# Optimization experiments

Measured on AMD Instinct MI355X. Metric: run time of the kernel, lower is better.

## Reference

```python
import jax, jax.numpy as jnp
import numpy as np

EPS = 1e-5
K_NN = 16

def _lin1d(x, W, b):
    # 1x1 Conv1d: x (B,C,N) -> (B,O,N)
    return jnp.einsum('oc,bcn->bon', W, x) + b[None, :, None]

def _lin2d(x, W, b):
    # 1x1 Conv2d: x (B,C,N,K) -> (B,O,N,K)
    return jnp.einsum('oc,bcnk->bonk', W, x) + b[None, :, None, None]

def _bn2d(x, gamma, beta):
    # train-mode BatchNorm2d over (B, N, K) per channel
    mean = jnp.mean(x, axis=(0, 2, 3), keepdims=True)
    var = jnp.var(x, axis=(0, 2, 3), keepdims=True)
    xh = (x - mean) * jax.lax.rsqrt(var + EPS)
    return gamma[None, :, None, None] * xh + beta[None, :, None, None]

def _knn_idx(pq, ps, k):
    # pq (B,3,N), ps (B,3,M) -> idx (B,N,K) of k nearest support points
    d2 = (jnp.sum(pq * pq, axis=1)[:, :, None]
          + jnp.sum(ps * ps, axis=1)[:, None, :]
          - 2.0 * jnp.einsum('bcn,bcm->bnm', pq, ps))
    _, idx = jax.lax.top_k(-d2, k)
    return idx

def _group(x, idx):
    # x (B,C,M), idx (B,N,K) -> (B,C,N,K)
    return jnp.take_along_axis(x[:, :, None, :], idx[:, None, :, :], axis=3)

def setup_inputs() -> dict:
    key = jax.random.key(0)
    ks = jax.random.split(key, 20)
    B, C, D, N, M, H = 4, 128, 64, 2048, 2048, 256
    s = lambda k, shape, scale: (jax.random.normal(k, shape, dtype=jnp.float32) * scale)
    return {
        'pq': s(ks[0], (B, 3, N), 1.0),
        'fq': s(ks[1], (B, C, N), 1.0),
        'ps': s(ks[2], (B, 3, M), 1.0),
        'fs': s(ks[3], (B, C, M), 1.0),
        'Wq': s(ks[4], (D, C), 0.05), 'bq': jnp.zeros((D,), jnp.float32),
        'Wk': s(ks[5], (D, C), 0.05), 'bk': jnp.zeros((D,), jnp.float32),
        'Wv': s(ks[6], (D, C), 0.05), 'bv': jnp.zeros((D,), jnp.float32),
        'Wp1': s(ks[7], (D, 3), 0.2), 'bp1': jnp.zeros((D,), jnp.float32),
        'gp': jnp.ones((D,), jnp.float32), 'btp': jnp.zeros((D,), jnp.float32),
        'Wp2': s(ks[8], (D, D), 0.05), 'bp2': jnp.zeros((D,), jnp.float32),
        'Wa1': s(ks[9], (H, D), 0.05), 'ba1': jnp.zeros((H,), jnp.float32),
        'ga': jnp.ones((H,), jnp.float32), 'bta': jnp.zeros((H,), jnp.float32),
        'Wa2': s(ks[10], (D, H), 0.05), 'ba2': jnp.zeros((D,), jnp.float32),
        'We': s(ks[11], (C, D), 0.05), 'be': jnp.zeros((C,), jnp.float32),
    }

def reference(pq, fq, ps, fs, Wq, bq, Wk, bk, Wv, bv,
              Wp1, bp1, gp, btp, Wp2, bp2,
              Wa1, ba1, ga, bta, Wa2, ba2, We, be):
    identity = fq
    q = _lin1d(fq, Wq, bq)          # (B,D,N)
    k = _lin1d(fs, Wk, bk)          # (B,D,M)
    v = _lin1d(fs, Wv, bv)          # (B,D,M)
    idx = _knn_idx(pq, ps, K_NN)    # (B,N,K)
    key_g = _group(k, idx)          # (B,D,N,K)
    qk_rel = q[:, :, :, None] - key_g
    pos_rel = pq[:, :, :, None] - _group(ps, idx)  # (B,3,N,K)
    # pos_mlp: conv-bn-relu-conv
    pe = _lin2d(pos_rel, Wp1, bp1)
    pe = jax.nn.relu(_bn2d(pe, gp, btp))
    pe = _lin2d(pe, Wp2, bp2)       # (B,D,N,K)
    # attn_mlp: conv-bn-relu-conv
    a = _lin2d(qk_rel + pe, Wa1, ba1)
    a = jax.nn.relu(_bn2d(a, ga, bta))
    a = _lin2d(a, Wa2, ba2)         # (B,D,N,K)
    attn = jax.nn.softmax(a, axis=-1)
    val = _group(v, idx) + pe       # (B,D,N,K)
    agg = jnp.einsum('bcnk,bcnk->bcn', attn, val)
    return _lin1d(agg, We, be) + identity
```

## Files before the change

### kernel.cpp

```cpp
#include <hip/hip_runtime.h>
#include <stdint.h>

#define NN 2048
#define MM 2048
#define NSAMP 131072

typedef float  fv4 __attribute__((ext_vector_type(4)));
typedef short  bfv8 __attribute__((ext_vector_type(8)));
typedef short  bfv4 __attribute__((ext_vector_type(4)));
typedef unsigned short u16;
typedef unsigned long long u64;

__device__ inline u16 f2bf(float x){
  unsigned u = __float_as_uint(x);
  return (u16)((u + 0x7FFFu + ((u>>16)&1u)) >> 16);
}
__device__ inline float bf2f(u16 u){ return __uint_as_float(((unsigned)u)<<16); }
#define MFMA16 __builtin_amdgcn_mfma_f32_16x16x32_bf16

__global__ __launch_bounds__(256) void k_prep(
    const float* __restrict__ Wq, const float* __restrict__ Wk, const float* __restrict__ Wv,
    const float* __restrict__ Wp2, const float* __restrict__ Wa2, const float* __restrict__ We,
    const float* __restrict__ ps,
    u16* __restrict__ Wqbf, u16* __restrict__ Wkbf, u16* __restrict__ Wvbf,
    u16* __restrict__ Wp2bf, u16* __restrict__ Wa2bf, u16* __restrict__ Webf,
    fv4* __restrict__ psP) {
  int gid = blockIdx.x * 256 + threadIdx.x;
  if (gid < 8192)  { Wqbf[gid] = f2bf(Wq[gid]); Wkbf[gid] = f2bf(Wk[gid]);
                     Wvbf[gid] = f2bf(Wv[gid]); Webf[gid] = f2bf(We[gid]); }
  if (gid < 4096)  Wp2bf[gid] = f2bf(Wp2[gid]);
  if (gid < 16384) Wa2bf[gid] = f2bf(Wa2[gid]);
  if (gid < 8192)  { int b = gid >> 11, m = gid & 2047;
    float x = ps[(b*3+0)*MM + m], y = ps[(b*3+1)*MM + m], z = ps[(b*3+2)*MM + m];
    fv4 p; p.x = x; p.y = y; p.z = z; p.w = x*x + y*y + z*z;
    psP[gid] = p; }
}

__global__ __launch_bounds__(256) void k_qkv(
    const float* __restrict__ fq, const float* __restrict__ fs,
    const u16* __restrict__ Wqbf, const u16* __restrict__ Wkbf, const u16* __restrict__ Wvbf,
    const float* __restrict__ bq, const float* __restrict__ bk, const float* __restrict__ bv,
    float* __restrict__ qT, float* __restrict__ kT, float* __restrict__ vT) {
  __shared__ u16 tile[2][32 * 136];
  int bid = blockIdx.x;
  int b = bid >> 6, p0 = (bid & 63) * 32;
  int t = threadIdx.x;
  int w = t >> 6, l = t & 63, lq = l >> 4, ln = l & 15;
  {
    int cq = t >> 3, n4 = (t & 7) * 4;
    #pragma unroll
    for (int it = 0; it < 4; ++it) {
      int c = it * 32 + cq;
      fv4 vq = *(const fv4*)&fq[(b*128 + c)*2048 + p0 + n4];
      fv4 vs = *(const fv4*)&fs[(b*128 + c)*2048 + p0 + n4];
      #pragma unroll
      for (int j = 0; j < 4; ++j) {
        tile[0][(n4 + j)*136 + c] = f2bf(vq[j]);
        tile[1][(n4 + j)*136 + c] = f2bf(vs[j]);
      }
    }
  }
  bfv8 A[3][4];
  #pragma unroll
  for (int mat = 0; mat < 3; ++mat) {
    const u16* W = mat == 0 ? Wqbf : (mat == 1 ? Wkbf : Wvbf);
    #pragma unroll
    for (int kk = 0; kk < 4; ++kk)
      A[mat][kk] = *(const bfv8*)(W + (w*16 + ln)*128 + kk*32 + lq*8);
  }
  __syncthreads();
  fv4 acc[3][2];
  #pragma unroll
  for (int mat = 0; mat < 3; ++mat) {
    const u16* tl = tile[mat == 0 ? 0 : 1];
    #pragma unroll
    for (int nt = 0; nt < 2; ++nt) {
      fv4 a = {0.f,0.f,0.f,0.f};
      #pragma unroll
      for (int kk = 0; kk < 4; ++kk) {
        bfv8 bb = *(const bfv8*)&tl[(nt*16 + ln)*136 + kk*32 + lq*8];
        a = MFMA16(A[mat][kk], bb, a, 0, 0, 0);
      }
      acc[mat][nt] = a;
    }
  }
  #pragma unroll
  for (int mat = 0; mat < 3; ++mat) {
    float* dst = mat == 0 ? qT : (mat == 1 ? kT : vT);
    const float* bia = mat == 0 ? bq : (mat == 1 ? bk : bv);
    fv4 bq4 = *(const fv4*)&bia[w*16 + lq*4];
    #pragma unroll
    for (int nt = 0; nt < 2; ++nt) {
      fv4 o = acc[mat][nt] + bq4;
      *(fv4*)&dst[(b*NN + p0 + nt*16 + ln)*64 + w*16 + lq*4] = o;
    }
  }
}

__global__ __launch_bounds__(128) void k_knn(
    const float* __restrict__ pq, const fv4* __restrict__ psP,
    int* __restrict__ idxb, float* __restrict__ posPart) {
  __shared__ u64 cand[2][64 * 17];
  __shared__ float sacc[2][9];
  int t = threadIdx.x, w = t >> 6, lane = t & 63;
  int qi = blockIdx.x * 2 + w;
  int b = qi >> 11, n = qi & 2047;
  const float* pqb = pq + b * 3 * NN;
  const fv4* psb = psP + b * 2048;
  float qx = pqb[n], qy = pqb[NN + n], qz = pqb[2 * NN + n];
  float qq = qx * qx + qy * qy + qz * qz;

  u64 A[16], Bv[16];
  #pragma unroll
  for (int j = 0; j < 16; ++j) {
    int m = lane + 64 * j;
    fv4 P = psb[m];
    float d2 = qq + P.w - 2.f * (qx * P.x + qy * P.y + qz * P.z);
    unsigned bu = __float_as_uint(d2);
    bu = (bu & 0x80000000u) ? ~bu : (bu | 0x80000000u);
    A[j] = (((u64)bu) << 32) | (unsigned)m;
  }
  #pragma unroll
  for (int j = 0; j < 16; ++j) {
    int m = lane + 64 * (j + 16);
    fv4 P = psb[m];
    float d2 = qq + P.w - 2.f * (qx * P.x + qy * P.y + qz * P.z);
    unsigned bu = __float_as_uint(d2);
    bu = (bu & 0x80000000u) ? ~bu : (bu | 0x80000000u);
    Bv[j] = (((u64)bu) << 32) | (unsigned)m;
  }
  #pragma unroll
  for (int k = 2; k <= 16; k <<= 1) {
    #pragma unroll
    for (int j = k >> 1; j > 0; j >>= 1) {
      #pragma unroll
      for (int i = 0; i < 16; ++i) {
        int l2 = i ^ j;
        if (l2 > i) {
          bool up = ((i & k) == 0);
          { u64 x = A[i], y = A[l2];
            bool sw = up ? (y < x) : (x < y);
            A[i] = sw ? y : x;  A[l2] = sw ? x : y; }
          { u64 x = Bv[i], y = Bv[l2];
            bool sw = up ? (y < x) : (x < y);
            Bv[i] = sw ? y : x; Bv[l2] = sw ? x : y; }
        }
      }
    }
  }
  #pragma unroll
  for (int i = 0; i < 16; ++i) {
    u64 y = Bv[15 - i];
    A[i] = A[i] < y ? A[i] : y;
  }
  #pragma unroll
  for (int j = 8; j > 0; j >>= 1) {
    #pragma unroll
    for (int i = 0; i < 16; ++i) {
      int l2 = i ^ j;
      if (l2 > i) {
        u64 x = A[i], y = A[l2];
        bool sw = (y < x);
        A[i] = sw ? y : x;  A[l2] = sw ? x : y;
      }
    }
  }
  #pragma unroll
  for (int i = 0; i < 16; ++i) cand[w][lane * 17 + i] = A[i];
  float s0=0.f,s1=0.f,s2=0.f,s3=0.f,s4=0.f,s5=0.f,s6=0.f,s7=0.f,s8=0.f;
  int head = 0;
  for (int r = 0; r < 16; ++r) {
    u64 v = (head < 16) ? cand[w][lane * 17 + head] : ~0ULL;
    u64 mv = v;
    #pragma unroll
    for (int off = 32; off > 0; off >>= 1) {
      u64 o = __shfl_xor(mv, off, 64);
      mv = o < mv ? o : mv;
    }
    if (v == mv) head++;
    unsigned m = (unsigned)(mv & 0xFFFFFFFFu);
    if (lane == 0) idxb[qi * 16 + r] = (int)m;
    fv4 P = psb[m];
    float r0 = qx - P.x, r1 = qy - P.y, r2 = qz - P.z;
    s0 += r0; s1 += r1; s2 += r2;
    s3 += r0*r0; s4 += r0*r1; s5 += r0*r2;
    s6 += r1*r1; s7 += r1*r2; s8 += r2*r2;
  }
  if (lane == 0) {
    sacc[w][0]=s0; sacc[w][1]=s1; sacc[w][2]=s2; sacc[w][3]=s3; sacc[w][4]=s4;
    sacc[w][5]=s5; sacc[w][6]=s6; sacc[w][7]=s7; sacc[w][8]=s8;
  }
  __syncthreads();
  if (t < 9) posPart[blockIdx.x * 12 + t] = sacc[0][t] + sacc[1][t];
}

__global__ __launch_bounds__(256) void k_posfinal(
    const float* __restrict__ Wp1, const float* __restrict__ bp1,
    const float* __restrict__ gp, const float* __restrict__ btp,
    const float* __restrict__ posPart, float* __restrict__ Wp1f, float* __restrict__ bp1f) {
  __shared__ float red[4][9];
  __shared__ float st[9];
  int t = threadIdx.x;
  int w = t >> 6, lane = t & 63;
  float s[9];
  #pragma unroll
  for (int i = 0; i < 9; ++i) s[i] = 0.f;
  #pragma unroll
  for (int it = 0; it < 16; ++it) {
    const float* p = posPart + (it * 256 + t) * 12;
    fv4 a = *(const fv4*)p;
    fv4 b4 = *(const fv4*)(p + 4);
    float c8 = p[8];
    s[0]+=a.x; s[1]+=a.y; s[2]+=a.z; s[3]+=a.w;
    s[4]+=b4.x; s[5]+=b4.y; s[6]+=b4.z; s[7]+=b4.w;
    s[8]+=c8;
  }
  #pragma unroll
  for (int off = 32; off > 0; off >>= 1)
    #pragma unroll
    for (int i = 0; i < 9; ++i) s[i] += __shfl_xor(s[i], off, 64);
  if (lane == 0)
    #pragma unroll
    for (int i = 0; i < 9; ++i) red[w][i] = s[i];
  __syncthreads();
  if (t < 9) st[t] = red[0][t] + red[1][t] + red[2][t] + red[3][t];
  __syncthreads();
  if (t < 64) {
    int d = t;
    const float invN = 1.f / (float)NSAMP;
    float m0 = st[0]*invN, m1 = st[1]*invN, m2 = st[2]*invN;
    float C00 = st[3]*invN - m0*m0, C01 = st[4]*invN - m0*m1, C02 = st[5]*invN - m0*m2;
    float C11 = st[6]*invN - m1*m1, C12 = st[7]*invN - m1*m2, C22 = st[8]*invN - m2*m2;
    float w0 = Wp1[d*3], w1 = Wp1[d*3+1], w2 = Wp1[d*3+2];
    float mean = w0*m0 + w1*m1 + w2*m2 + bp1[d];
    float var = w0*w0*C00 + w1*w1*C11 + w2*w2*C22 + 2.f*(w0*w1*C01 + w0*w2*C02 + w1*w2*C12);
    float scale = gp[d] * rsqrtf(var + 1e-5f);
    Wp1f[d*3]   = scale * w0;
    Wp1f[d*3+1] = scale * w1;
    Wp1f[d*3+2] = scale * w2;
    bp1f[d] = btp[d] + scale * (bp1[d] - mean);
  }
}

__global__ __launch_bounds__(256) void k_ystats(
    const float* __restrict__ pq, const float* __restrict__ ps,
    const float* __restrict__ qT, const float* __restrict__ kT,
    const int* __restrict__ idxb,
    const float* __restrict__ Wp1f, const float* __restrict__ bp1f,
    const u16* __restrict__ Wp2bf, const float* __restrict__ bp2,
    float* __restrict__ Gpart, float* __restrict__ ySumPart) {
  __shared__ __align__(16) unsigned char smem[21760];
  u16*   hp   = (u16*)smem;
  u16*   y2   = (u16*)(smem + 9216);
  float* r3   = (float*)(smem + 18432);
  float* qc   = (float*)(smem + 19200);
  int*   idxA = (int*)(smem + 20224);
  float* sWp1 = (float*)(smem + 20480);
  float* sbp1 = (float*)(smem + 21248);
  float* sbp2 = (float*)(smem + 21504);

  const int t = threadIdx.x;
  const int w = t >> 6, l = t & 63, lq = l >> 4, ln = l & 15;
  const int d0 = 16*w + lq*4;

  if (t < 192) sWp1[t] = Wp1f[t];
  if (t < 64){ sbp1[t] = bp1f[t]; sbp2[t] = bp2[t]; }

  bfv8 Ape[2];
  #pragma unroll
  for (int kk = 0; kk < 2; ++kk)
    Ape[kk] = *(const bfv8*)(Wp2bf + (16*w + ln)*64 + kk*32 + lq*8);

  fv4 gacc[4];
  #pragma unroll
  for (int nt = 0; nt < 4; ++nt) gacc[nt] = (fv4){0.f,0.f,0.f,0.f};
  float ys[4] = {0.f, 0.f, 0.f, 0.f};
  __syncthreads();

  for (int ch = 0; ch < 4; ++ch) {
    const int p0 = blockIdx.x * 16 + ch * 4;
    const int b  = p0 >> 11;
    const int bN = b * 2048;
    if (t < 64) idxA[t] = idxb[p0*16 + t];
    qc[t] = qT[(p0 + (t>>6))*64 + (t & 63)];
    __syncthreads();
    if (t < 192) { int c = t >> 6, s = t & 63; int n = (p0 + (s>>4)) & 2047;
      r3[c*64 + s] = pq[(b*3+c)*NN + n] - ps[(b*3+c)*MM + idxA[s]]; }
    __syncthreads();
    { int s = t >> 2, iq = t & 3;
      float r0 = r3[s], r1 = r3[64+s], r2 = r3[128+s];
      u16 tmp[16];
      #pragma unroll
      for (int e = 0; e < 16; ++e) { int i = iq*16 + e;
        float v = sbp1[i] + sWp1[i*3]*r0 + sWp1[i*3+1]*r1 + sWp1[i*3+2]*r2;
        tmp[e] = f2bf(fmaxf(v, 0.f)); }
      *(bfv8*)&hp[s*72 + iq*16]     = *(const bfv8*)&tmp[0];
      *(bfv8*)&hp[s*72 + iq*16 + 8] = *(const bfv8*)&tmp[8];
    }
    __syncthreads();
    {
      fv4 pe[4];
      #pragma unroll
      for (int nt = 0; nt < 4; ++nt) {
        fv4 acc = {0.f,0.f,0.f,0.f};
        #pragma unroll
        for (int kk = 0; kk < 2; ++kk) {
          bfv8 bb = *(const bfv8*)&hp[(nt*16 + ln)*72 + kk*32 + lq*8];
          acc = MFMA16(Ape[kk], bb, acc, 0, 0, 0);
        }
        pe[nt] = acc;
      }
      fv4 bp2q = *(const fv4*)&sbp2[d0];
      #pragma unroll
      for (int nt = 0; nt < 4; ++nt) {
        int s = nt*16 + ln;
        int mi = idxA[s];
        fv4 kg = *(const fv4*)(kT + (bN + mi)*64 + d0);
        fv4 qv = *(const fv4*)&qc[nt*64 + d0];
        fv4 yv = qv - kg + pe[nt] + bp2q;
        #pragma unroll
        for (int r = 0; r < 4; ++r) { y2[(d0 + r)*72 + s] = f2bf(yv[r]); ys[r] += yv[r]; }
      }
    }
    __syncthreads();
    #pragma unroll
    for (int kk = 0; kk < 2; ++kk) {
      bfv8 aa = *(const bfv8*)&y2[(16*w + ln)*72 + kk*32 + lq*8];
      #pragma unroll
      for (int nt = 0; nt < 4; ++nt) {
        bfv8 bb = *(const bfv8*)&y2[(nt*16 + ln)*72 + kk*32 + lq*8];
        gacc[nt] = MFMA16(aa, bb, gacc[nt], 0, 0, 0);
      }
    }
    __syncthreads();
  }
  #pragma unroll
  for (int nt = 0; nt < 4; ++nt)
    #pragma unroll
    for (int r = 0; r < 4; ++r)
      Gpart[blockIdx.x*4096 + (16*w + lq*4 + r)*64 + nt*16 + ln] = gacc[nt][r];
  #pragma unroll
  for (int off = 1; off <= 8; off <<= 1) {
    #pragma unroll
    for (int r = 0; r < 4; ++r) ys[r] += __shfl_xor(ys[r], off, 64);
  }
  if (ln == 0) {
    #pragma unroll
    for (int r = 0; r < 4; ++r) ySumPart[blockIdx.x*64 + d0 + r] = ys[r];
  }
}

__global__ __launch_bounds__(256) void k_gred(
    const float* __restrict__ Gpart, const float* __restrict__ ySumPart,
    float* __restrict__ G, float* __restrict__ ySum) {
  int bid = blockIdx.x, t = threadIdx.x;
  if (bid < 16) {
    int j = bid*256 + t;
    float s = 0.f;
    for (int p = 0; p < 512; ++p) s += Gpart[p*4096 + j];
    G[j] = s;
  } else if (t < 64) {
    float s = 0.f;
    for (int p = 0; p < 512; ++p) s += ySumPart[p*64 + t];
    ySum[t] = s;
  }
}

__global__ __launch_bounds__(256) void k_attnfinal(
    const float* __restrict__ Wa1, const float* __restrict__ ba1,
    const float* __restrict__ ga, const float* __restrict__ bta,
    const float* __restrict__ ySum, const float* __restrict__ G,
    u16* __restrict__ Wa1fbf, float* __restrict__ ba1f) {
  __shared__ float red[256];
  __shared__ float mu[64];
  __shared__ float sc[1];
  int h = blockIdx.x, t = threadIdx.x;
  const float invN = 1.f / (float)NSAMP;
  if (t < 64) mu[t] = ySum[t] * invN;
  __syncthreads();
  float acc = 0.f;
  #pragma unroll
  for (int e = 0; e < 16; ++e) {
    int pi = t*16 + e, i = pi >> 6, j = pi & 63;
    float cov = G[pi]*invN - mu[i]*mu[j];
    acc += Wa1[h*64 + i] * Wa1[h*64 + j] * cov;
  }
  red[t] = acc;
  __syncthreads();
  for (int s = 128; s > 0; s >>= 1) { if (t < s) red[t] += red[t + s]; __syncthreads(); }
  float var = red[0];
  __syncthreads();
  red[t] = (t < 64) ? Wa1[h*64 + t] * mu[t] : 0.f;
  __syncthreads();
  for (int s = 128; s > 0; s >>= 1) { if (t < s) red[t] += red[t + s]; __syncthreads(); }
  if (t == 0) {
    float mean  = red[0] + ba1[h];
    float scale = ga[h] * rsqrtf(var + 1e-5f);
    sc[0] = scale;
    ba1f[h] = bta[h] + scale * (ba1[h] - mean);
  }
  __syncthreads();
  if (t < 64) Wa1fbf[h*64 + t] = f2bf(sc[0] * Wa1[h*64 + t]);
}

__global__ __launch_bounds__(256) void k_main(
    const float* __restrict__ pq, const float* __restrict__ ps,
    const float* __restrict__ qT, const float* __restrict__ kT, const float* __restrict__ vT,
    const int* __restrict__ idxb,
    const float* __restrict__ Wp1f, const float* __restrict__ bp1f,
    const u16* __restrict__ Wp2bf, const float* __restrict__ bp2,
    const u16* __restrict__ Wa1fbf, const float* __restrict__ ba1f,
    const u16* __restrict__ Wa2bf, const float* __restrict__ ba2,
    const u16* __restrict__ Webf, const float* __restrict__ be,
    const float* __restrict__ fq,
    u16* __restrict__ aggbf, float* __restrict__ out) {
  __shared__ __align__(16) unsigned char smem[65024];
  u16*   hp   = (u16*)smem;
  u16*   ha   = (u16*)smem;
  u16*   ylds = (u16*)(smem + 33792);
  float* at   = (float*)(smem + 33792);
  u16*   vt   = (u16*)(smem + 51200);
  float* r3   = (float*)(smem + 60416);
  float* qc   = (float*)(smem + 61184);
  int*   idxA = (int*)(smem + 62208);
  float* sWp1 = (float*)(smem + 62464);
  float* sbp1 = (float*)(smem + 63232);
  float* sbp2 = (float*)(smem + 63488);
  float* sba1 = (float*)(smem + 63744);
  float* sba2 = (float*)(smem + 64768);

  const int t = threadIdx.x;
  const int w = t >> 6, l = t & 63, lq = l >> 4, ln = l & 15;
  const int d0 = 16*w + lq*4;

  if (t < 192) sWp1[t] = Wp1f[t];
  if (t < 64){ sbp1[t] = bp1f[t]; sbp2[t] = bp2[t]; sba2[t] = ba2[t]; }
  sba1[t] = ba1f[t];

  bfv8 Ape[2], A1[4][2], A2[8];
  #pragma unroll
  for (int kk = 0; kk < 2; ++kk)
    Ape[kk] = *(const bfv8*)(Wp2bf + (16*w + ln)*64 + kk*32 + lq*8);
  #pragma unroll
  for (int mt = 0; mt < 4; ++mt)
    #pragma unroll
    for (int kk = 0; kk < 2; ++kk)
      A1[mt][kk] = *(const bfv8*)(Wa1fbf + (64*w + mt*16 + ln)*64 + kk*32 + lq*8);
  #pragma unroll
  for (int kk = 0; kk < 8; ++kk)
    A2[kk] = *(const bfv8*)(Wa2bf + (16*w + ln)*256 + kk*32 + lq*8);
  __syncthreads();

  for (int ch = 0; ch < 4; ++ch) {
    const int p0 = blockIdx.x * 16 + ch * 4;
    const int b  = p0 >> 11;
    const int bN = b * 2048;
    if (t < 64) idxA[t] = idxb[p0*16 + t];
    qc[t] = qT[(p0 + (t>>6))*64 + (t & 63)];
    __syncthreads();
    if (t < 192) { int c = t >> 6, s = t & 63; int n = (p0 + (s>>4)) & 2047;
      r3[c*64 + s] = pq[(b*3+c)*NN + n] - ps[(b*3+c)*MM + idxA[s]]; }
    __syncthreads();
    { int s = t >> 2, iq = t & 3;
      float r0 = r3[s], r1 = r3[64+s], r2 = r3[128+s];
      u16 tmp[16];
      #pragma unroll
      for (int e = 0; e < 16; ++e) { int i = iq*16 + e;
        float v = sbp1[i] + sWp1[i*3]*r0 + sWp1[i*3+1]*r1 + sWp1[i*3+2]*r2;
        tmp[e] = f2bf(fmaxf(v, 0.f)); }
      *(bfv8*)&hp[s*72 + iq*16]     = *(const bfv8*)&tmp[0];
      *(bfv8*)&hp[s*72 + iq*16 + 8] = *(const bfv8*)&tmp[8];
    }
    __syncthreads();
    {
      fv4 pe[4];
      #pragma unroll
      for (int nt = 0; nt < 4; ++nt) {
        fv4 acc = {0.f,0.f,0.f,0.f};
        #pragma unroll
        for (int kk = 0; kk < 2; ++kk) {
          bfv8 bb = *(const bfv8*)&hp[(nt*16 + ln)*72 + kk*32 + lq*8];
          acc = MFMA16(Ape[kk], bb, acc, 0, 0, 0);
        }
        pe[nt] = acc;
      }
      fv4 bp2q = *(const fv4*)&sbp2[d0];
      #pragma unroll
      for (int nt = 0; nt < 4; ++nt) {
        int s = nt*16 + ln;
        int mi = idxA[s];
        fv4 kg = *(const fv4*)(kT + (bN + mi)*64 + d0);
        fv4 vg = *(const fv4*)(vT + (bN + mi)*64 + d0);
        fv4 qv = *(const fv4*)&qc[nt*64 + d0];
        fv4 pv = pe[nt] + bp2q;
        fv4 yv = qv - kg + pv;
        fv4 vv = vg + pv;
        u16 yp[4], vp[4];
        #pragma unroll
        for (int r = 0; r < 4; ++r) { yp[r] = f2bf(yv[r]); vp[r] = f2bf(vv[r]); }
        *(bfv4*)&ylds[s*72 + d0] = *(const bfv4*)yp;
        *(bfv4*)&vt[s*72 + d0]   = *(const bfv4*)vp;
      }
    }
    __syncthreads();
    #pragma unroll
    for (int nt = 0; nt < 4; ++nt) {
      int s = nt*16 + ln;
      bfv8 b0 = *(const bfv8*)&ylds[s*72 + lq*8];
      bfv8 b1 = *(const bfv8*)&ylds[s*72 + 32 + lq*8];
      #pragma unroll
      for (int mt = 0; mt < 4; ++mt) {
        fv4 acc = {0.f,0.f,0.f,0.f};
        acc = MFMA16(A1[mt][0], b0, acc, 0, 0, 0);
        acc = MFMA16(A1[mt][1], b1, acc, 0, 0, 0);
        int h0 = 64*w + mt*16 + lq*4;
        fv4 bq = *(const fv4*)&sba1[h0];
        u16 hv[4];
        #pragma unroll
        for (int r = 0; r < 4; ++r) hv[r] = f2bf(fmaxf(acc[r] + bq[r], 0.f));
        *(bfv4*)&ha[s*264 + h0] = *(const bfv4*)hv;
      }
    }
    __syncthreads();
    {
      fv4 acc2[4];
      #pragma unroll
      for (int nt = 0; nt < 4; ++nt) acc2[nt] = (fv4){0.f,0.f,0.f,0.f};
      #pragma unroll
      for (int kk = 0; kk < 8; ++kk) {
        #pragma unroll
        for (int nt = 0; nt < 4; ++nt) {
          bfv8 bb = *(const bfv8*)&ha[(nt*16 + ln)*264 + kk*32 + lq*8];
          acc2[nt] = MFMA16(A2[kk], bb, acc2[nt], 0, 0, 0);
        }
      }
      fv4 ba2q = *(const fv4*)&sba2[d0];
      #pragma unroll
      for (int nt = 0; nt < 4; ++nt) {
        int s = nt*16 + ln;
        fv4 o = acc2[nt] + ba2q;
        *(fv4*)&at[s*68 + d0] = o;
      }
    }
    __syncthreads();
    {
      int dd = t & 63, pt = t >> 6;
      float a[16];
      #pragma unroll
      for (int k = 0; k < 16; ++k) a[k] = at[(pt*16 + k)*68 + dd];
      float mx = a[0];
      #pragma unroll
      for (int k = 1; k < 16; ++k) mx = fmaxf(mx, a[k]);
      float sum = 0.f, num = 0.f;
      #pragma unroll
      for (int k = 0; k < 16; ++k) {
        float e = __expf(a[k] - mx);
        sum += e;
        num += e * bf2f(vt[(pt*16 + k)*72 + dd]);
      }
      aggbf[(p0 + pt)*64 + dd] = f2bf(num / sum);
    }
    __syncthreads();
  }
  {
    const int P0 = blockIdx.x * 16;
    const int b  = P0 >> 11;
    const int n0 = P0 & 2047;
    bfv8 EA[2][2];
    #pragma unroll
    for (int mt = 0; mt < 2; ++mt)
      #pragma unroll
      for (int kk = 0; kk < 2; ++kk)
        EA[mt][kk] = *(const bfv8*)(Webf + ((w*2 + mt)*16 + ln)*64 + kk*32 + lq*8);
    const u16* bp = aggbf + (P0 + ln)*64;
    bfv8 b0 = *(const bfv8*)(bp + lq*8);
    bfv8 b1 = *(const bfv8*)(bp + 32 + lq*8);
    fv4 eacc[2];
    #pragma unroll
    for (int mt = 0; mt < 2; ++mt) {
      fv4 a = {0.f,0.f,0.f,0.f};
      a = MFMA16(EA[mt][0], b0, a, 0, 0, 0);
      a = MFMA16(EA[mt][1], b1, a, 0, 0, 0);
      eacc[mt] = a;
    }
    #pragma unroll
    for (int mt = 0; mt < 2; ++mt) {
      int c0 = (w*2 + mt)*16 + lq*4;
      fv4 bev = *(const fv4*)&be[c0];
      #pragma unroll
      for (int r = 0; r < 4; ++r) {
        int c = c0 + r;
        int o = (b*128 + c)*2048 + n0 + ln;
        out[o] = eacc[mt][r] + bev[r] + fq[o];
      }
    }
  }
}

extern "C" void kernel_launch(void* const* d_in, const int* in_sizes, int n_in,
                              void* d_out, int out_size, void* d_ws, size_t ws_size,
                              hipStream_t stream) {
  (void)in_sizes; (void)n_in; (void)out_size; (void)ws_size;
  const float* pq  = (const float*)d_in[0];
  const float* fq  = (const float*)d_in[1];
  const float* ps  = (const float*)d_in[2];
  const float* fs  = (const float*)d_in[3];
  const float* Wq  = (const float*)d_in[4];  const float* bq  = (const float*)d_in[5];
  const float* Wk  = (const float*)d_in[6];  const float* bk  = (const float*)d_in[7];
  const float* Wv  = (const float*)d_in[8];  const float* bv  = (const float*)d_in[9];
  const float* Wp1 = (const float*)d_in[10]; const float* bp1 = (const float*)d_in[11];
  const float* gp  = (const float*)d_in[12]; const float* btp = (const float*)d_in[13];
  const float* Wp2 = (const float*)d_in[14]; const float* bp2 = (const float*)d_in[15];
  const float* Wa1 = (const float*)d_in[16]; const float* ba1 = (const float*)d_in[17];
  const float* ga  = (const float*)d_in[18]; const float* bta = (const float*)d_in[19];
  const float* Wa2 = (const float*)d_in[20]; const float* ba2 = (const float*)d_in[21];
  const float* We  = (const float*)d_in[22]; const float* be  = (const float*)d_in[23];
  float* ws = (float*)d_ws;
  float* qT    = ws;
  float* kT    = ws + 524288;
  float* vT    = ws + 1048576;
  u16*   aggbf = (u16*)(ws + 1572864);
  int*   idxb  = (int*)(ws + 2097152);
  u16*   Wqbf  = (u16*)(ws + 2228224);
  u16*   Wkbf  = (u16*)(ws + 2232320);
  u16*   Wvbf  = (u16*)(ws + 2236416);
  u16*   Webf  = (u16*)(ws + 2240512);
  fv4*   psP   = (fv4*)(ws + 2244608);
  float* Wp1f  = ws + 2375680;
  float* bp1f  = ws + 2375872;
  float* ba1f  = ws + 2375936;
  float* G     = ws + 2376192;
  float* ySum  = ws + 2380288;
  float* ySumP = ws + 2380352;
  u16*   Wp2bf  = (u16*)(ws + 2413120);
  u16*   Wa2bf  = (u16*)(ws + 2415168);
  u16*   Wa1fbf = (u16*)(ws + 2423360);
  float* posPart = ws + 2431552;
  float* Gpart   = ws + 2480704;
  float* out   = (float*)d_out;

  k_prep<<<64, 256, 0, stream>>>(Wq, Wk, Wv, Wp2, Wa2, We, ps,
                                 Wqbf, Wkbf, Wvbf, Wp2bf, Wa2bf, Webf, psP);
  k_qkv<<<256, 256, 0, stream>>>(fq, fs, Wqbf, Wkbf, Wvbf, bq, bk, bv, qT, kT, vT);
  k_knn<<<4096, 128, 0, stream>>>(pq, psP, idxb, posPart);
  k_posfinal<<<1, 256, 0, stream>>>(Wp1, bp1, gp, btp, posPart, Wp1f, bp1f);
  k_ystats<<<512, 256, 0, stream>>>(pq, ps, qT, kT, idxb, Wp1f, bp1f, Wp2bf, bp2,
                                    Gpart, ySumP);
  k_gred<<<17, 256, 0, stream>>>(Gpart, ySumP, G, ySum);
  k_attnfinal<<<256, 256, 0, stream>>>(Wa1, ba1, ga, bta, ySum, G, Wa1fbf, ba1f);
  k_main<<<512, 256, 0, stream>>>(pq, ps, qT, kT, vT, idxb, Wp1f, bp1f, Wp2bf, bp2,
                                  Wa1fbf, ba1f, Wa2bf, ba2, Webf, be, fq, aggbf, out);
}
```

Measured before the change: 244.6 us.

## Merge prep, QKV projection and KNN into one block-specialized kernel

Fuses the weight-conversion, QKV projection and KNN kernels into a single launch that dispatches on block index. QKV now converts its weights to bf16 inline, and KNN reads planar support coordinates directly and recomputes squared norms instead of using a packed buffer. KNN blocks now hold four queries instead of two, which halves the posPart partials. The goal is to cut two launches and their serialization gaps and let the independent stages overlap, at the cost of redundant per-block weight conversion and more scattered coordinate loads in KNN.

```diff
diff --git a/kernel.cpp b/kernel.cpp
--- a/kernel.cpp
+++ b/kernel.cpp
@@ -18,180 +18,188 @@
 __device__ inline float bf2f(u16 u){ return __uint_as_float(((unsigned)u)<<16); }
 #define MFMA16 __builtin_amdgcn_mfma_f32_16x16x32_bf16
 
-__global__ __launch_bounds__(256) void k_prep(
+__global__ __launch_bounds__(256) void k_front(
+    const float* __restrict__ pq, const float* __restrict__ ps,
+    const float* __restrict__ fq, const float* __restrict__ fs,
     const float* __restrict__ Wq, const float* __restrict__ Wk, const float* __restrict__ Wv,
     const float* __restrict__ Wp2, const float* __restrict__ Wa2, const float* __restrict__ We,
-    const float* __restrict__ ps,
-    u16* __restrict__ Wqbf, u16* __restrict__ Wkbf, u16* __restrict__ Wvbf,
+    const float* __restrict__ bq, const float* __restrict__ bk, const float* __restrict__ bv,
     u16* __restrict__ Wp2bf, u16* __restrict__ Wa2bf, u16* __restrict__ Webf,
-    fv4* __restrict__ psP) {
-  int gid = blockIdx.x * 256 + threadIdx.x;
-  if (gid < 8192)  { Wqbf[gid] = f2bf(Wq[gid]); Wkbf[gid] = f2bf(Wk[gid]);
-                     Wvbf[gid] = f2bf(Wv[gid]); Webf[gid] = f2bf(We[gid]); }
-  if (gid < 4096)  Wp2bf[gid] = f2bf(Wp2[gid]);
-  if (gid < 16384) Wa2bf[gid] = f2bf(Wa2[gid]);
-  if (gid < 8192)  { int b = gid >> 11, m = gid & 2047;
-    float x = ps[(b*3+0)*MM + m], y = ps[(b*3+1)*MM + m], z = ps[(b*3+2)*MM + m];
-    fv4 p; p.x = x; p.y = y; p.z = z; p.w = x*x + y*y + z*z;
-    psP[gid] = p; }
-}
-
-__global__ __launch_bounds__(256) void k_qkv(
-    const float* __restrict__ fq, const float* __restrict__ fs,
-    const u16* __restrict__ Wqbf, const u16* __restrict__ Wkbf, const u16* __restrict__ Wvbf,
-    const float* __restrict__ bq, const float* __restrict__ bk, const float* __restrict__ bv,
-    float* __restrict__ qT, float* __restrict__ kT, float* __restrict__ vT) {
-  __shared__ u16 tile[2][32 * 136];
-  int bid = blockIdx.x;
-  int b = bid >> 6, p0 = (bid & 63) * 32;
-  int t = threadIdx.x;
-  int w = t >> 6, l = t & 63, lq = l >> 4, ln = l & 15;
+    float* __restrict__ qT, float* __restrict__ kT, float* __restrict__ vT,
+    int* __restrict__ idxb, float* __restrict__ posPart) {
+  __shared__ __align__(16) unsigned char smem[35072];
+  const int bid = blockIdx.x;
+  const int t = threadIdx.x;
+
+  if (bid < 64) {
+    int gid = bid * 256 + t;
+    if (gid < 4096)  Wp2bf[gid] = f2bf(Wp2[gid]);
+    if (gid < 16384) Wa2bf[gid] = f2bf(Wa2[gid]);
+    if (gid < 8192)  Webf[gid]  = f2bf(We[gid]);
+    return;
+  }
+
+  if (bid < 320) {
+    u16* tile0 = (u16*)smem;
+    u16* tile1 = (u16*)(smem + 8704);
+    int r = bid - 64;
+    int b = r >> 6, p0 = (r & 63) * 32;
+    int w = t >> 6, l = t & 63, lq = l >> 4, ln = l & 15;
+    {
+      int cq = t >> 3, n4 = (t & 7) * 4;
+      #pragma unroll
+      for (int it = 0; it < 4; ++it) {
+        int c = it * 32 + cq;
+        fv4 vq = *(const fv4*)&fq[(b*128 + c)*2048 + p0 + n4];
+        fv4 vs = *(const fv4*)&fs[(b*128 + c)*2048 + p0 + n4];
+        #pragma unroll
+        for (int j = 0; j < 4; ++j) {
+          tile0[(n4 + j)*136 + c] = f2bf(vq[j]);
+          tile1[(n4 + j)*136 + c] = f2bf(vs[j]);
+        }
+      }
+    }
+    bfv8 A[3][4];
+    #pragma unroll
+    for (int mat = 0; mat < 3; ++mat) {
+      const float* Wf = mat == 0 ? Wq : (mat == 1 ? Wk : Wv);
+      #pragma unroll
+      for (int kk = 0; kk < 4; ++kk) {
+        const float* src = Wf + (w*16 + ln)*128 + kk*32 + lq*8;
+        fv4 a0 = *(const fv4*)src, a1 = *(const fv4*)(src + 4);
+        u16 tmp[8];
+        #pragma unroll
+        for (int e = 0; e < 4; ++e) { tmp[e] = f2bf(a0[e]); tmp[4+e] = f2bf(a1[e]); }
+        A[mat][kk] = *(const bfv8*)tmp;
+      }
+    }
+    __syncthreads();
+    fv4 acc[3][2];
+    #pragma unroll
+    for (int mat = 0; mat < 3; ++mat) {
+      const u16* tl = mat == 0 ? tile0 : tile1;
+      #pragma unroll
+      for (int nt = 0; nt < 2; ++nt) {
+        fv4 a = {0.f,0.f,0.f,0.f};
+        #pragma unroll
+        for (int kk = 0; kk < 4; ++kk) {
+          bfv8 bb = *(const bfv8*)&tl[(nt*16 + ln)*136 + kk*32 + lq*8];
+          a = MFMA16(A[mat][kk], bb, a, 0, 0, 0);
+        }
+        acc[mat][nt] = a;
+      }
+    }
+    #pragma unroll
+    for (int mat = 0; mat < 3; ++mat) {
+      float* dst = mat == 0 ? qT : (mat == 1 ? kT : vT);
+      const float* bia = mat == 0 ? bq : (mat == 1 ? bk : bv);
+      fv4 bq4 = *(const fv4*)&bia[w*16 + lq*4];
+      #pragma unroll
+      for (int nt = 0; nt < 2; ++nt) {
+        fv4 o = acc[mat][nt] + bq4;
+        *(fv4*)&dst[(b*NN + p0 + nt*16 + ln)*64 + w*16 + lq*4] = o;
+      }
+    }
+    return;
+  }
+
   {
-    int cq = t >> 3, n4 = (t & 7) * 4;
-    #pragma unroll
-    for (int it = 0; it < 4; ++it) {
-      int c = it * 32 + cq;
-      fv4 vq = *(const fv4*)&fq[(b*128 + c)*2048 + p0 + n4];
-      fv4 vs = *(const fv4*)&fs[(b*128 + c)*2048 + p0 + n4];
-      #pragma unroll
-      for (int j = 0; j < 4; ++j) {
-        tile[0][(n4 + j)*136 + c] = f2bf(vq[j]);
-        tile[1][(n4 + j)*136 + c] = f2bf(vs[j]);
-      }
-    }
-  }
-  bfv8 A[3][4];
-  #pragma unroll
-  for (int mat = 0; mat < 3; ++mat) {
-    const u16* W = mat == 0 ? Wqbf : (mat == 1 ? Wkbf : Wvbf);
-    #pragma unroll
-    for (int kk = 0; kk < 4; ++kk)
-      A[mat][kk] = *(const bfv8*)(W + (w*16 + ln)*128 + kk*32 + lq*8);
-  }
-  __syncthreads();
-  fv4 acc[3][2];
-  #pragma unroll
-  for (int mat = 0; mat < 3; ++mat) {
-    const u16* tl = tile[mat == 0 ? 0 : 1];
-    #pragma unroll
-    for (int nt = 0; nt < 2; ++nt) {
-      fv4 a = {0.f,0.f,0.f,0.f};
-      #pragma unroll
-      for (int kk = 0; kk < 4; ++kk) {
-        bfv8 bb = *(const bfv8*)&tl[(nt*16 + ln)*136 + kk*32 + lq*8];
-        a = MFMA16(A[mat][kk], bb, a, 0, 0, 0);
-      }
-      acc[mat][nt] = a;
-    }
-  }
-  #pragma unroll
-  for (int mat = 0; mat < 3; ++mat) {
-    float* dst = mat == 0 ? qT : (mat == 1 ? kT : vT);
-    const float* bia = mat == 0 ? bq : (mat == 1 ? bk : bv);
-    fv4 bq4 = *(const fv4*)&bia[w*16 + lq*4];
-    #pragma unroll
-    for (int nt = 0; nt < 2; ++nt) {
-      fv4 o = acc[mat][nt] + bq4;
-      *(fv4*)&dst[(b*NN + p0 + nt*16 + ln)*64 + w*16 + lq*4] = o;
-    }
-  }
-}
-
-__global__ __launch_bounds__(128) void k_knn(
-    const float* __restrict__ pq, const fv4* __restrict__ psP,
-    int* __restrict__ idxb, float* __restrict__ posPart) {
-  __shared__ u64 cand[2][64 * 17];
-  __shared__ float sacc[2][9];
-  int t = threadIdx.x, w = t >> 6, lane = t & 63;
-  int qi = blockIdx.x * 2 + w;
-  int b = qi >> 11, n = qi & 2047;
-  const float* pqb = pq + b * 3 * NN;
-  const fv4* psb = psP + b * 2048;
-  float qx = pqb[n], qy = pqb[NN + n], qz = pqb[2 * NN + n];
-  float qq = qx * qx + qy * qy + qz * qz;
-
-  u64 A[16], Bv[16];
-  #pragma unroll
-  for (int j = 0; j < 16; ++j) {
-    int m = lane + 64 * j;
-    fv4 P = psb[m];
-    float d2 = qq + P.w - 2.f * (qx * P.x + qy * P.y + qz * P.z);
-    unsigned bu = __float_as_uint(d2);
-    bu = (bu & 0x80000000u) ? ~bu : (bu | 0x80000000u);
-    A[j] = (((u64)bu) << 32) | (unsigned)m;
-  }
-  #pragma unroll
-  for (int j = 0; j < 16; ++j) {
-    int m = lane + 64 * (j + 16);
-    fv4 P = psb[m];
-    float d2 = qq + P.w - 2.f * (qx * P.x + qy * P.y + qz * P.z);
-    unsigned bu = __float_as_uint(d2);
-    bu = (bu & 0x80000000u) ? ~bu : (bu | 0x80000000u);
-    Bv[j] = (((u64)bu) << 32) | (unsigned)m;
-  }
-  #pragma unroll
-  for (int k = 2; k <= 16; k <<= 1) {
-    #pragma unroll
-    for (int j = k >> 1; j > 0; j >>= 1) {
+    u64*   cand = (u64*)smem;
+    float* sacc = (float*)(smem + 34816);
+    int w = t >> 6, lane = t & 63;
+    int blk = bid - 320;
+    int qi = blk * 4 + w;
+    int b = qi >> 11, n = qi & 2047;
+    const float* pqb = pq + b * 3 * NN;
+    const float* psb = ps + b * 3 * MM;
+    float qx = pqb[n], qy = pqb[NN + n], qz = pqb[2 * NN + n];
+    float qq = qx * qx + qy * qy + qz * qz;
+
+    u64 A[16], Bv[16];
+    #pragma unroll
+    for (int j = 0; j < 16; ++j) {
+      int m = lane + 64 * j;
+      float sx = psb[m], sy = psb[MM + m], sz = psb[2 * MM + m];
+      float ss  = sx * sx + sy * sy + sz * sz;
+      float d2 = qq + ss - 2.f * (qx * sx + qy * sy + qz * sz);
+      unsigned bu = __float_as_uint(d2);
+      bu = (bu & 0x80000000u) ? ~bu : (bu | 0x80000000u);
+      A[j] = (((u64)bu) << 32) | (unsigned)m;
+    }
+    #pragma unroll
+    for (int j = 0; j < 16; ++j) {
+      int m = lane + 64 * (j + 16);
+      float sx = psb[m], sy = psb[MM + m], sz = psb[2 * MM + m];
+      float ss  = sx * sx + sy * sy + sz * sz;
+      float d2 = qq + ss - 2.f * (qx * sx + qy * sy + qz * sz);
+      unsigned bu = __float_as_uint(d2);
+      bu = (bu & 0x80000000u) ? ~bu : (bu | 0x80000000u);
+      Bv[j] = (((u64)bu) << 32) | (unsigned)m;
+    }
+    #pragma unroll
+    for (int k = 2; k <= 16; k <<= 1) {
+      #pragma unroll
+      for (int j = k >> 1; j > 0; j >>= 1) {
+        #pragma unroll
+        for (int i = 0; i < 16; ++i) {
+          int l2 = i ^ j;
+          if (l2 > i) {
+            bool up = ((i & k) == 0);
+            { u64 x = A[i], y = A[l2];
+              bool sw = up ? (y < x) : (x < y);
+              A[i] = sw ? y : x;  A[l2] = sw ? x : y; }
+            { u64 x = Bv[i], y = Bv[l2];
+              bool sw = up ? (y < x) : (x < y);
+              Bv[i] = sw ? y : x; Bv[l2] = sw ? x : y; }
+          }
+        }
+      }
+    }
+    #pragma unroll
+    for (int i = 0; i < 16; ++i) {
+      u64 y = Bv[15 - i];
+      A[i] = A[i] < y ? A[i] : y;
+    }
+    #pragma unroll
+    for (int j = 8; j > 0; j >>= 1) {
       #pragma unroll
       for (int i = 0; i < 16; ++i) {
         int l2 = i ^ j;
         if (l2 > i) {
-          bool up = ((i & k) == 0);
-          { u64 x = A[i], y = A[l2];
-            bool sw = up ? (y < x) : (x < y);
-            A[i] = sw ? y : x;  A[l2] = sw ? x : y; }
-          { u64 x = Bv[i], y = Bv[l2];
-            bool sw = up ? (y < x) : (x < y);
-            Bv[i] = sw ? y : x; Bv[l2] = sw ? x : y; }
+          u64 x = A[i], y = A[l2];
+          bool sw = (y < x);
+          A[i] = sw ? y : x;  A[l2] = sw ? x : y;
         }
       }
     }
-  }
-  #pragma unroll
-  for (int i = 0; i < 16; ++i) {
-    u64 y = Bv[15 - i];
-    A[i] = A[i] < y ? A[i] : y;
-  }
-  #pragma unroll
-  for (int j = 8; j > 0; j >>= 1) {
-    #pragma unroll
-    for (int i = 0; i < 16; ++i) {
-      int l2 = i ^ j;
-      if (l2 > i) {
-        u64 x = A[i], y = A[l2];
-        bool sw = (y < x);
-        A[i] = sw ? y : x;  A[l2] = sw ? x : y;
-      }
-    }
-  }
-  #pragma unroll
-  for (int i = 0; i < 16; ++i) cand[w][lane * 17 + i] = A[i];
-  float s0=0.f,s1=0.f,s2=0.f,s3=0.f,s4=0.f,s5=0.f,s6=0.f,s7=0.f,s8=0.f;
-  int head = 0;
-  for (int r = 0; r < 16; ++r) {
-    u64 v = (head < 16) ? cand[w][lane * 17 + head] : ~0ULL;
-    u64 mv = v;
-    #pragma unroll
-    for (int off = 32; off > 0; off >>= 1) {
-      u64 o = __shfl_xor(mv, off, 64);
-      mv = o < mv ? o : mv;
-    }
-    if (v == mv) head++;
-    unsigned m = (unsigned)(mv & 0xFFFFFFFFu);
-    if (lane == 0) idxb[qi * 16 + r] = (int)m;
-    fv4 P = psb[m];
-    float r0 = qx - P.x, r1 = qy - P.y, r2 = qz - P.z;
-    s0 += r0; s1 += r1; s2 += r2;
-    s3 += r0*r0; s4 += r0*r1; s5 += r0*r2;
-    s6 += r1*r1; s7 += r1*r2; s8 += r2*r2;
-  }
-  if (lane == 0) {
-    sacc[w][0]=s0; sacc[w][1]=s1; sacc[w][2]=s2; sacc[w][3]=s3; sacc[w][4]=s4;
-    sacc[w][5]=s5; sacc[w][6]=s6; sacc[w][7]=s7; sacc[w][8]=s8;
-  }
-  __syncthreads();
-  if (t < 9) posPart[blockIdx.x * 12 + t] = sacc[0][t] + sacc[1][t];
+    #pragma unroll
+    for (int i = 0; i < 16; ++i) cand[w*1088 + lane*17 + i] = A[i];
+    float s0=0.f,s1=0.f,s2=0.f,s3=0.f,s4=0.f,s5=0.f,s6=0.f,s7=0.f,s8=0.f;
+    int head = 0;
+    for (int r = 0; r < 16; ++r) {
+      u64 v = (head < 16) ? cand[w*1088 + lane*17 + head] : ~0ULL;
+      u64 mv = v;
+      #pragma unroll
+      for (int off = 32; off > 0; off >>= 1) {
+        u64 o = __shfl_xor(mv, off, 64);
+        mv = o < mv ? o : mv;
+      }
+      if (v == mv) head++;
+      unsigned m = (unsigned)(mv & 0xFFFFFFFFu);
+      if (lane == 0) idxb[qi * 16 + r] = (int)m;
+      float r0 = qx - psb[m], r1 = qy - psb[MM + m], r2 = qz - psb[2*MM + m];
+      s0 += r0; s1 += r1; s2 += r2;
+      s3 += r0*r0; s4 += r0*r1; s5 += r0*r2;
+      s6 += r1*r1; s7 += r1*r2; s8 += r2*r2;
+    }
+    if (lane == 0) {
+      sacc[w*9+0]=s0; sacc[w*9+1]=s1; sacc[w*9+2]=s2; sacc[w*9+3]=s3; sacc[w*9+4]=s4;
+      sacc[w*9+5]=s5; sacc[w*9+6]=s6; sacc[w*9+7]=s7; sacc[w*9+8]=s8;
+    }
+    __syncthreads();
+    if (t < 9) posPart[blk * 12 + t] =
+        sacc[t] + sacc[9 + t] + sacc[18 + t] + sacc[27 + t];
+  }
 }
 
 __global__ __launch_bounds__(256) void k_posfinal(
@@ -206,7 +214,7 @@
   #pragma unroll
   for (int i = 0; i < 9; ++i) s[i] = 0.f;
   #pragma unroll
-  for (int it = 0; it < 16; ++it) {
+  for (int it = 0; it < 8; ++it) {
     const float* p = posPart + (it * 256 + t) * 12;
     fv4 a = *(const fv4*)p;
     fv4 b4 = *(const fv4*)(p + 4);
@@ -621,11 +629,6 @@
   float* vT    = ws + 1048576;
   u16*   aggbf = (u16*)(ws + 1572864);
   int*   idxb  = (int*)(ws + 2097152);
-  u16*   Wqbf  = (u16*)(ws + 2228224);
-  u16*   Wkbf  = (u16*)(ws + 2232320);
-  u16*   Wvbf  = (u16*)(ws + 2236416);
-  u16*   Webf  = (u16*)(ws + 2240512);
-  fv4*   psP   = (fv4*)(ws + 2244608);
   float* Wp1f  = ws + 2375680;
   float* bp1f  = ws + 2375872;
   float* ba1f  = ws + 2375936;
@@ -635,14 +638,14 @@
   u16*   Wp2bf  = (u16*)(ws + 2413120);
   u16*   Wa2bf  = (u16*)(ws + 2415168);
   u16*   Wa1fbf = (u16*)(ws + 2423360);
-  float* posPart = ws + 2431552;
-  float* Gpart   = ws + 2480704;
+  u16*   Webf   = (u16*)(ws + 2431552);
+  float* posPart = ws + 2435648;
+  float* Gpart   = ws + 2460224;
   float* out   = (float*)d_out;
 
-  k_prep<<<64, 256, 0, stream>>>(Wq, Wk, Wv, Wp2, Wa2, We, ps,
-                                 Wqbf, Wkbf, Wvbf, Wp2bf, Wa2bf, Webf, psP);
-  k_qkv<<<256, 256, 0, stream>>>(fq, fs, Wqbf, Wkbf, Wvbf, bq, bk, bv, qT, kT, vT);
-  k_knn<<<4096, 128, 0, stream>>>(pq, psP, idxb, posPart);
+  k_front<<<2368, 256, 0, stream>>>(pq, ps, fq, fs, Wq, Wk, Wv, Wp2, Wa2, We,
+                                    bq, bk, bv, Wp2bf, Wa2bf, Webf,
+                                    qT, kT, vT, idxb, posPart);
   k_posfinal<<<1, 256, 0, stream>>>(Wp1, bp1, gp, btp, posPart, Wp1f, bp1f);
   k_ystats<<<512, 256, 0, stream>>>(pq, ps, qT, kT, idxb, Wp1f, bp1f, Wp2bf, bp2,
                                     Gpart, ySumP);
```

Result: no change. 246.6 us (+0.8%).
